# Performance work log

Measured on AMD Instinct MI355X. Metric: run time of the kernel, lower is better.

Reference implementation:

```python
import jax, jax.numpy as jnp
import numpy as np

B, T, D = 4, 2048, 1024
H, DK, DV = 16, 64, 64


def setup_inputs() -> dict:
    key = jax.random.key(0)
    ks = jax.random.split(key, 12)
    std = 1.0 / np.sqrt(D)
    inp = {
        "query": jax.random.normal(ks[0], (B, T, D), jnp.float32),
        "key": jax.random.normal(ks[1], (B, T, D), jnp.float32),
        "value": jax.random.normal(ks[2], (B, T, D), jnp.float32),
        "mask": jnp.ones((B, 1, 1, T), dtype=bool),
        # weights stored as [in, out] (torch Linear applies x @ W.T + b)
        "Wq": jax.random.truncated_normal(ks[3], -2, 2, (D, H * DK), jnp.float32) * std,
        "bq": jnp.zeros((H * DK,), jnp.float32),
        "Wk": jax.random.truncated_normal(ks[4], -2, 2, (D, H * DK), jnp.float32) * std,
        "bk": jnp.zeros((H * DK,), jnp.float32),
        "Wv": jax.random.truncated_normal(ks[5], -2, 2, (D, H * DV), jnp.float32) * std,
        "bv": jnp.zeros((H * DV,), jnp.float32),
        "Wo": jax.random.truncated_normal(ks[6], -2, 2, (H * DV, D), jnp.float32) * (1.0 / np.sqrt(H * DV)),
        "bo": jnp.zeros((D,), jnp.float32),
    }
    return inp


def reference(query, key, value, mask, Wq, bq, Wk, bk, Wv, bv, Wo, bo):
    denom = 1.0 / np.sqrt(DK)
    q = (query @ Wq + bq).reshape(B, T, H, DK)
    k = (key @ Wk + bk).reshape(B, T, H, DK)
    v = (value @ Wv + bv).reshape(B, T, H, DV)
    # [B, H, T, T] attention logits
    logits = jnp.einsum("bthd,bThd->bhtT", q, k) * denom
    logits = jnp.where(mask, logits, -1e30)
    w = jax.nn.softmax(logits, axis=-1)
    attn = jnp.einsum("bhtT,bThd->bthd", w, v).reshape(B, T, H * DV)
    return attn @ Wo + bo
```

## Files before the change

kernel.cpp:

```cpp
#include <hip/hip_runtime.h>


typedef _Float16 f16;
typedef f16 f16x4 __attribute__((ext_vector_type(4)));
typedef f16 f16x8 __attribute__((ext_vector_type(8)));
typedef __fp16 h16x2 __attribute__((ext_vector_type(2)));
typedef float f32x4 __attribute__((ext_vector_type(4)));
typedef float f32x16 __attribute__((ext_vector_type(16)));

__device__ __forceinline__ void gload_lds16(const void* g, void* l) {
  __builtin_amdgcn_global_load_lds(
      (const __attribute__((address_space(1))) unsigned int*)g,
      (__attribute__((address_space(3))) unsigned int*)l, 16, 0, 0);
}

__device__ __forceinline__ unsigned pku(float a, float b) {
  h16x2 p = __builtin_amdgcn_cvt_pkrtz(a, b);
  return __builtin_bit_cast(unsigned, p);
}

__device__ __forceinline__ f16x8 cvt8(const f32x4& a, const f32x4& b) {
  union { unsigned u[4]; f16x8 v; } m;
  m.u[0] = pku(a[0], a[1]);
  m.u[1] = pku(a[2], a[3]);
  m.u[2] = pku(b[0], b[1]);
  m.u[3] = pku(b[2], b[3]);
  return m.v;
}

__global__ __launch_bounds__(256) void wtrans4(const float* __restrict__ W0,
                                               const float* __restrict__ W1,
                                               const float* __restrict__ W2,
                                               const float* __restrict__ W3,
                                               f16* __restrict__ D0,
                                               f16* __restrict__ D1,
                                               f16* __restrict__ D2,
                                               f16* __restrict__ D3) {
  __shared__ float tile[32][33];
  const float* W;
  f16* D;
  switch (blockIdx.z) {
    case 0: W = W0; D = D0; break;
    case 1: W = W1; D = D1; break;
    case 2: W = W2; D = D2; break;
    default: W = W3; D = D3; break;
  }
  int tx = threadIdx.x, ty = threadIdx.y;
  int o0 = blockIdx.x * 32, i0 = blockIdx.y * 32;
#pragma unroll
  for (int r = 0; r < 32; r += 8)
    tile[ty + r][tx] = W[(size_t)(i0 + ty + r) * 1024 + o0 + tx];
  __syncthreads();
#pragma unroll
  for (int r = 0; r < 32; r += 8)
    D[(size_t)(o0 + ty + r) * 1024 + i0 + tx] = (f16)tile[tx][ty + r];
}

__global__ __launch_bounds__(256) void gemm_proj(
    const float* __restrict__ Aq, const float* __restrict__ Ak,
    const float* __restrict__ Av, const f16* __restrict__ WTq,
    const f16* __restrict__ WTk, const f16* __restrict__ WTv,
    const float* __restrict__ bq, const float* __restrict__ bk,
    const float* __restrict__ bv, f16* __restrict__ QB, f16* __restrict__ KB,
    f16* __restrict__ VT) {
  constexpr int N = 1024, K = 1024;
  constexpr int BM = 128, BK = 32;
  __shared__ f16 As[BM * BK];
  __shared__ f16 Bs[BM * BK];

  const int big = blockIdx.x;
  const int seg = big >> 9;
  const int bid = big & 511;
  const float* A;
  const f16* Bt;
  const float* bias;
  f16* C;
  if (seg == 0) { A = Aq; Bt = WTq; bias = bq; C = QB; }
  else if (seg == 1) { A = Ak; Bt = WTk; bias = bk; C = KB; }
  else { A = Av; Bt = WTv; bias = bv; C = VT; }
  const bool vmode = (seg == 2);

  const int t = threadIdx.x;
  int swz = (bid & 7) * 64 + (bid >> 3);
  const int tm = swz >> 3, tn = swz & 7;

  const int lane = t & 63, w = t >> 6;
  const int wr = w >> 1, wc = w & 1;
  const int lrow = lane & 15, kgrp = lane >> 4;

  f32x4 zero4 = {0.f, 0.f, 0.f, 0.f};
  f32x4 acc[4][4];
#pragma unroll
  for (int mi = 0; mi < 4; ++mi)
#pragma unroll
    for (int ni = 0; ni < 4; ++ni) acc[mi][ni] = zero4;

  const int srow = t >> 2;
  const int scol = (t & 3) * 8;
  const float* Ag32 = A + (size_t)(tm * BM + srow) * K + scol;
  const f16* Bg = Bt + (size_t)(tn * BM + srow) * K + scol;
  f16* Asl = &As[t * 8];
  f16* Bsl = &Bs[t * 8];

  f32x4 ar[4];
  auto loadA = [&](int k0) {
    ar[0] = *(const f32x4*)(Ag32 + k0);
    ar[1] = *(const f32x4*)(Ag32 + k0 + 4);
    ar[2] = *(const f32x4*)(Ag32 + (size_t)64 * K + k0);
    ar[3] = *(const f32x4*)(Ag32 + (size_t)64 * K + k0 + 4);
  };

  loadA(0);
  for (int k0 = 0; k0 < K; k0 += BK) {
    __syncthreads();
    *(f16x8*)Asl = cvt8(ar[0], ar[1]);
    *(f16x8*)(Asl + 64 * BK) = cvt8(ar[2], ar[3]);
    gload_lds16(Bg + k0, Bsl);
    gload_lds16(Bg + k0 + (size_t)64 * K, Bsl + 64 * BK);
    __syncthreads();
    if (k0 + BK < K) loadA(k0 + BK);

    f16x8 af[4], bf[4];
#pragma unroll
    for (int mi = 0; mi < 4; ++mi)
      af[mi] = *(const f16x8*)&As[(wr * 64 + mi * 16 + lrow) * BK + kgrp * 8];
#pragma unroll
    for (int ni = 0; ni < 4; ++ni)
      bf[ni] = *(const f16x8*)&Bs[(wc * 64 + ni * 16 + lrow) * BK + kgrp * 8];
#pragma unroll
    for (int mi = 0; mi < 4; ++mi)
#pragma unroll
      for (int ni = 0; ni < 4; ++ni)
        acc[mi][ni] = __builtin_amdgcn_mfma_f32_16x16x32_f16(af[mi], bf[ni],
                                                             acc[mi][ni], 0, 0, 0);
  }

#pragma unroll
  for (int mi = 0; mi < 4; ++mi) {
#pragma unroll
    for (int ni = 0; ni < 4; ++ni) {
      int col = tn * BM + wc * 64 + ni * 16 + lrow;
      float bv_ = bias[col];
#pragma unroll
      for (int j = 0; j < 4; ++j) {
        int row = tm * BM + wr * 64 + mi * 16 + kgrp * 4 + j;
        float v = acc[mi][ni][j] + bv_;
        if (vmode) {
          int bb = row >> 11, tt = row & 2047;
          C[((size_t)(bb * 1024 + col)) * 2048 + tt] = (f16)v;
        } else {
          C[(size_t)row * N + col] = (f16)v;
        }
      }
    }
  }
}

__global__ __launch_bounds__(256) void gemm_out(const f16* __restrict__ A,
                                                const f16* __restrict__ Bt,
                                                const float* __restrict__ bias,
                                                float* __restrict__ C32) {
  constexpr int N = 1024, K = 1024;
  constexpr int BM = 128, BK = 32;
  __shared__ f16 As[BM * BK];
  __shared__ f16 Bs[BM * BK];

  const int t = threadIdx.x;
  int bid = blockIdx.x;
  int swz = (bid & 7) * 64 + (bid >> 3);
  const int tm = swz >> 3, tn = swz & 7;

  const int lane = t & 63, w = t >> 6;
  const int wr = w >> 1, wc = w & 1;
  const int lrow = lane & 15, kgrp = lane >> 4;

  f32x4 zero4 = {0.f, 0.f, 0.f, 0.f};
  f32x4 acc[4][4];
#pragma unroll
  for (int mi = 0; mi < 4; ++mi)
#pragma unroll
    for (int ni = 0; ni < 4; ++ni) acc[mi][ni] = zero4;

  const int srow = t >> 2;
  const int scol = (t & 3) * 8;
  const f16* Ag = A + (size_t)(tm * BM + srow) * K + scol;
  const f16* Bg = Bt + (size_t)(tn * BM + srow) * K + scol;
  f16* Asl = &As[t * 8];
  f16* Bsl = &Bs[t * 8];

  for (int k0 = 0; k0 < K; k0 += BK) {
    __syncthreads();
    gload_lds16(Ag + k0, Asl);
    gload_lds16(Ag + k0 + (size_t)64 * K, Asl + 64 * BK);
    gload_lds16(Bg + k0, Bsl);
    gload_lds16(Bg + k0 + (size_t)64 * K, Bsl + 64 * BK);
    __syncthreads();

    f16x8 af[4], bf[4];
#pragma unroll
    for (int mi = 0; mi < 4; ++mi)
      af[mi] = *(const f16x8*)&As[(wr * 64 + mi * 16 + lrow) * BK + kgrp * 8];
#pragma unroll
    for (int ni = 0; ni < 4; ++ni)
      bf[ni] = *(const f16x8*)&Bs[(wc * 64 + ni * 16 + lrow) * BK + kgrp * 8];
#pragma unroll
    for (int mi = 0; mi < 4; ++mi)
#pragma unroll
      for (int ni = 0; ni < 4; ++ni)
        acc[mi][ni] = __builtin_amdgcn_mfma_f32_16x16x32_f16(af[mi], bf[ni],
                                                             acc[mi][ni], 0, 0, 0);
  }

#pragma unroll
  for (int mi = 0; mi < 4; ++mi) {
#pragma unroll
    for (int ni = 0; ni < 4; ++ni) {
      int col = tn * BM + wc * 64 + ni * 16 + lrow;
      float bv = bias[col];
#pragma unroll
      for (int j = 0; j < 4; ++j) {
        int row = tm * BM + wr * 64 + mi * 16 + kgrp * 4 + j;
        C32[(size_t)row * N + col] = acc[mi][ni][j] + bv;
      }
    }
  }
}

__global__ __launch_bounds__(256) void attn_fwd(const f16* __restrict__ Q,
                                                const f16* __restrict__ Kc,
                                                const f16* __restrict__ Vt,
                                                f16* __restrict__ O) {
  constexpr int T = 2048, HD = 1024;
  __shared__ __align__(16) f16 lds[16384];
  char* LB = (char*)lds;

  const int t = threadIdx.x;
  const int lane = t & 63, w = t >> 6;
  const int q5 = lane & 31, hi = lane >> 5;
  const int r7 = q5 & 7;
  int bid = blockIdx.x;
  int swzb = (bid & 7) * 128 + (bid >> 3);
  const int qt = swzb & 15, h = (swzb >> 4) & 15, b = swzb >> 8;

  f16x8 aq[4];
  {
    const f16* qp =
        Q + (size_t)(b * T + qt * 128 + w * 32 + q5) * HD + h * 64 + hi * 8;
#pragma unroll
    for (int s = 0; s < 4; ++s)
      aq[s] = (*(const f16x8*)(qp + s * 16)) * (f16)0.18033688f;
  }

  float m_r = -INFINITY, l_r = 0.f;
  f32x16 z16 = {0.f};
  f32x16 oa0 = z16, oa1 = z16;

  unsigned koff[4];
#pragma unroll
  for (int s = 0; s < 4; ++s)
    koff[s] = q5 * 128 + (((2 * s + hi) ^ r7) << 4);

  const int l8 = lane & 7, lr8 = lane >> 3;
  const int cs = (l8 ^ lr8) * 8;
  const f16* kg0 = Kc + (size_t)(b * T + w * 16 + lr8) * HD + h * 64 + cs;
  const f16* kg1 = kg0 + (size_t)8 * HD;
  const f16* vg0 = Vt + (size_t)(b * 1024 + h * 64 + w * 16 + lr8) * T + cs;
  const f16* vg1 = vg0 + (size_t)8 * T;
  const unsigned dsto = w * 2048 + lane * 16;

  auto stage = [&](unsigned sb) {
    gload_lds16(kg0, LB + sb + dsto);
    gload_lds16(kg1, LB + sb + dsto + 1024);
    gload_lds16(vg0, LB + 16384 + sb + dsto);
    gload_lds16(vg1, LB + 16384 + sb + dsto + 1024);
    kg0 += (size_t)64 * HD; kg1 += (size_t)64 * HD;
    vg0 += 64; vg1 += 64;
  };

  auto mk = [&](float e0, float e1, float e2, float e3, float e4, float e5,
                float e6, float e7) -> f16x8 {
    unsigned A01 = pku(e0, e1), A23 = pku(e2, e3);
    unsigned B01 = pku(e4, e5), B23 = pku(e6, e7);
    unsigned X0 = hi ? A01 : B01;
    unsigned X1 = hi ? A23 : B23;
    unsigned R0 = (unsigned)__shfl_xor((int)X0, 32, 64);
    unsigned R1 = (unsigned)__shfl_xor((int)X1, 32, 64);
    union { unsigned u[4]; f16x8 v; } m;
    m.u[0] = hi ? R0 : A01;
    m.u[1] = hi ? R1 : A23;
    m.u[2] = hi ? B01 : R0;
    m.u[3] = hi ? B23 : R1;
    return m.v;
  };

  auto body = [&](unsigned rb, unsigned sb, bool doStage) {
    if (doStage) stage(sb);

    f32x16 s0 = z16, s1 = z16;
    __builtin_amdgcn_s_setprio(1);
#pragma unroll
    for (int s = 0; s < 4; ++s) {
      f16x8 ka = *(const f16x8*)(LB + (rb + koff[s]));
      f16x8 kb = *(const f16x8*)(LB + (rb + 4096 + koff[s]));
      s0 = __builtin_amdgcn_mfma_f32_32x32x16_f16(ka, aq[s], s0, 0, 0, 0);
      s1 = __builtin_amdgcn_mfma_f32_32x32x16_f16(kb, aq[s], s1, 0, 0, 0);
    }
    __builtin_amdgcn_s_setprio(0);

    float a0 = fmaxf(fmaxf(s0[0], s0[1]), fmaxf(s0[2], s0[3]));
    float a1 = fmaxf(fmaxf(s0[4], s0[5]), fmaxf(s0[6], s0[7]));
    float a2 = fmaxf(fmaxf(s0[8], s0[9]), fmaxf(s0[10], s0[11]));
    float a3 = fmaxf(fmaxf(s0[12], s0[13]), fmaxf(s0[14], s0[15]));
    float a4 = fmaxf(fmaxf(s1[0], s1[1]), fmaxf(s1[2], s1[3]));
    float a5 = fmaxf(fmaxf(s1[4], s1[5]), fmaxf(s1[6], s1[7]));
    float a6 = fmaxf(fmaxf(s1[8], s1[9]), fmaxf(s1[10], s1[11]));
    float a7 = fmaxf(fmaxf(s1[12], s1[13]), fmaxf(s1[14], s1[15]));
    float mx = fmaxf(fmaxf(fmaxf(a0, a1), fmaxf(a2, a3)),
                     fmaxf(fmaxf(a4, a5), fmaxf(a6, a7)));
    mx = fmaxf(mx, __shfl_xor(mx, 32, 64));
    if (__any(mx > m_r + 8.f)) {
      float mnew = fmaxf(m_r, mx);
      float sc = exp2f(m_r - mnew);
      l_r *= sc;
      m_r = mnew;
#pragma unroll
      for (int i = 0; i < 16; ++i) { oa0[i] *= sc; oa1[i] *= sc; }
    }
#pragma unroll
    for (int i = 0; i < 16; ++i) s0[i] = exp2f(s0[i] - m_r);
#pragma unroll
    for (int i = 0; i < 16; ++i) s1[i] = exp2f(s1[i] - m_r);
    float r0 = ((s0[0] + s0[1]) + (s0[2] + s0[3])) +
               ((s0[4] + s0[5]) + (s0[6] + s0[7]));
    float r1 = ((s0[8] + s0[9]) + (s0[10] + s0[11])) +
               ((s0[12] + s0[13]) + (s0[14] + s0[15]));
    float r2 = ((s1[0] + s1[1]) + (s1[2] + s1[3])) +
               ((s1[4] + s1[5]) + (s1[6] + s1[7]));
    float r3 = ((s1[8] + s1[9]) + (s1[10] + s1[11])) +
               ((s1[12] + s1[13]) + (s1[14] + s1[15]));
    float rs = (r0 + r1) + (r2 + r3);
    rs += __shfl_xor(rs, 32, 64);
    l_r += rs;

    f16x8 pb0 = mk(s0[0], s0[1], s0[2], s0[3], s0[4], s0[5], s0[6], s0[7]);
    f16x8 pb1 = mk(s0[8], s0[9], s0[10], s0[11], s0[12], s0[13], s0[14], s0[15]);
    f16x8 pb2 = mk(s1[0], s1[1], s1[2], s1[3], s1[4], s1[5], s1[6], s1[7]);
    f16x8 pb3 = mk(s1[8], s1[9], s1[10], s1[11], s1[12], s1[13], s1[14], s1[15]);

    __builtin_amdgcn_s_setprio(1);
    {
      f16x8 v0 = *(const f16x8*)(LB + (16384 + rb + koff[0]));
      f16x8 v1 = *(const f16x8*)(LB + (16384 + rb + 4096 + koff[0]));
      oa0 = __builtin_amdgcn_mfma_f32_32x32x16_f16(v0, pb0, oa0, 0, 0, 0);
      oa1 = __builtin_amdgcn_mfma_f32_32x32x16_f16(v1, pb0, oa1, 0, 0, 0);
      v0 = *(const f16x8*)(LB + (16384 + rb + koff[1]));
      v1 = *(const f16x8*)(LB + (16384 + rb + 4096 + koff[1]));
      oa0 = __builtin_amdgcn_mfma_f32_32x32x16_f16(v0, pb1, oa0, 0, 0, 0);
      oa1 = __builtin_amdgcn_mfma_f32_32x32x16_f16(v1, pb1, oa1, 0, 0, 0);
      v0 = *(const f16x8*)(LB + (16384 + rb + koff[2]));
      v1 = *(const f16x8*)(LB + (16384 + rb + 4096 + koff[2]));
      oa0 = __builtin_amdgcn_mfma_f32_32x32x16_f16(v0, pb2, oa0, 0, 0, 0);
      oa1 = __builtin_amdgcn_mfma_f32_32x32x16_f16(v1, pb2, oa1, 0, 0, 0);
      v0 = *(const f16x8*)(LB + (16384 + rb + koff[3]));
      v1 = *(const f16x8*)(LB + (16384 + rb + 4096 + koff[3]));
      oa0 = __builtin_amdgcn_mfma_f32_32x32x16_f16(v0, pb3, oa0, 0, 0, 0);
      oa1 = __builtin_amdgcn_mfma_f32_32x32x16_f16(v1, pb3, oa1, 0, 0, 0);
    }
    __builtin_amdgcn_s_setprio(0);

    __syncthreads();
  };

  stage(0);
  __syncthreads();

#pragma unroll 1
  for (int i = 0; i < 15; ++i) {
    body(0, 8192, true);
    body(8192, 0, true);
  }
  body(0, 8192, true);
  body(8192, 0, false);

  float inv = 1.f / l_r;
  f16* orow = O + (size_t)(b * T + qt * 128 + w * 32 + q5) * HD + h * 64;
#pragma unroll
  for (int t2 = 0; t2 < 2; ++t2) {
    const f32x16& oa = t2 ? oa1 : oa0;
#pragma unroll
    for (int j = 0; j < 4; ++j) {
      f16x4 ov;
      ov[0] = (f16)(oa[4 * j + 0] * inv);
      ov[1] = (f16)(oa[4 * j + 1] * inv);
      ov[2] = (f16)(oa[4 * j + 2] * inv);
      ov[3] = (f16)(oa[4 * j + 3] * inv);
      *(f16x4*)(orow + t2 * 32 + j * 8 + hi * 4) = ov;
    }
  }
}

extern "C" void kernel_launch(void* const* d_in, const int* in_sizes, int n_in,
                              void* d_out, int out_size, void* d_ws, size_t ws_size,
                              hipStream_t stream) {
  (void)in_sizes; (void)n_in; (void)out_size; (void)ws_size;
  const float* query = (const float*)d_in[0];
  const float* key   = (const float*)d_in[1];
  const float* value = (const float*)d_in[2];
  const float* Wq = (const float*)d_in[4];
  const float* bq = (const float*)d_in[5];
  const float* Wk = (const float*)d_in[6];
  const float* bk = (const float*)d_in[7];
  const float* Wv = (const float*)d_in[8];
  const float* bv = (const float*)d_in[9];
  const float* Wo = (const float*)d_in[10];
  const float* bo = (const float*)d_in[11];
  float* out = (float*)d_out;

  f16* ws  = (f16*)d_ws;
  f16* WTq = ws;
  f16* WTk = WTq + 1048576;
  f16* WTv = WTk + 1048576;
  f16* WTo = WTv + 1048576;
  f16* QB  = WTo + 1048576;
  f16* KB  = QB + 8388608;
  f16* VT  = KB + 8388608;
  f16* AB  = VT + 8388608;

  wtrans4<<<dim3(32, 32, 4), dim3(32, 8), 0, stream>>>(Wq, Wk, Wv, Wo,
                                                       WTq, WTk, WTv, WTo);
  gemm_proj<<<dim3(1536), dim3(256), 0, stream>>>(query, key, value,
                                                  WTq, WTk, WTv,
                                                  bq, bk, bv, QB, KB, VT);
  attn_fwd<<<dim3(1024), dim3(256), 0, stream>>>(QB, KB, VT, AB);
  gemm_out<<<dim3(512), dim3(256), 0, stream>>>(AB, WTo, bo, out);
}
```

Measured before the change: 261.1 us.

## Widen attention blocks to 512 threads and compute row sums via MFMA

The attention kernel now runs 8 waves per block over 256 query rows, so each staged K/V tile in LDS is shared by twice as many waves, and each thread issues half as many global-to-LDS loads. The softmax row sum moves from VALU adds plus a cross-lane shuffle to an MFMA against a ones vector, which accumulates the sum in the matrix unit. Max reduction uses three-input max chains, and exp2 calls the raw hardware intrinsic. The costs are extra MFMA work per iteration, a 16-float accumulator for the sum, and half as many blocks in the grid.

New measurement: 222.7 us. 14.7% less time.

```diff
diff --git a/kernel.cpp b/kernel.cpp
--- a/kernel.cpp
+++ b/kernel.cpp
@@ -26,6 +26,13 @@
   m.u[2] = pku(b[0], b[1]);
   m.u[3] = pku(b[2], b[3]);
   return m.v;
+}
+
+__device__ __forceinline__ float e2(float x) {
+  return __builtin_amdgcn_exp2f(x);
+}
+__device__ __forceinline__ float m3(float a, float b, float c) {
+  return fmaxf(fmaxf(a, b), c);
 }
 
 __global__ __launch_bounds__(256) void wtrans4(const float* __restrict__ W0,
@@ -226,10 +233,10 @@
   }
 }
 
-__global__ __launch_bounds__(256) void attn_fwd(const f16* __restrict__ Q,
-                                                const f16* __restrict__ Kc,
-                                                const f16* __restrict__ Vt,
-                                                f16* __restrict__ O) {
+__global__ __launch_bounds__(512, 4) void attn_fwd(const f16* __restrict__ Q,
+                                                   const f16* __restrict__ Kc,
+                                                   const f16* __restrict__ Vt,
+                                                   f16* __restrict__ O) {
   constexpr int T = 2048, HD = 1024;
   __shared__ __align__(16) f16 lds[16384];
   char* LB = (char*)lds;
@@ -239,21 +246,26 @@
   const int q5 = lane & 31, hi = lane >> 5;
   const int r7 = q5 & 7;
   int bid = blockIdx.x;
-  int swzb = (bid & 7) * 128 + (bid >> 3);
-  const int qt = swzb & 15, h = (swzb >> 4) & 15, b = swzb >> 8;
+  int swzb = (bid & 7) * 64 + (bid >> 3);
+  const int qt = swzb & 7, h = (swzb >> 3) & 15, b = swzb >> 7;
 
   f16x8 aq[4];
   {
     const f16* qp =
-        Q + (size_t)(b * T + qt * 128 + w * 32 + q5) * HD + h * 64 + hi * 8;
+        Q + (size_t)(b * T + qt * 256 + w * 32 + q5) * HD + h * 64 + hi * 8;
 #pragma unroll
     for (int s = 0; s < 4; ++s)
       aq[s] = (*(const f16x8*)(qp + s * 16)) * (f16)0.18033688f;
   }
 
-  float m_r = -INFINITY, l_r = 0.f;
+  float m_r = -INFINITY;
   f32x16 z16 = {0.f};
   f32x16 oa0 = z16, oa1 = z16;
+  f32x16 la = z16;
+
+  f16x8 ones;
+#pragma unroll
+  for (int i = 0; i < 8; ++i) ones[i] = (f16)1.f;
 
   unsigned koff[4];
 #pragma unroll
@@ -262,19 +274,15 @@
 
   const int l8 = lane & 7, lr8 = lane >> 3;
   const int cs = (l8 ^ lr8) * 8;
-  const f16* kg0 = Kc + (size_t)(b * T + w * 16 + lr8) * HD + h * 64 + cs;
-  const f16* kg1 = kg0 + (size_t)8 * HD;
-  const f16* vg0 = Vt + (size_t)(b * 1024 + h * 64 + w * 16 + lr8) * T + cs;
-  const f16* vg1 = vg0 + (size_t)8 * T;
-  const unsigned dsto = w * 2048 + lane * 16;
+  const f16* kg = Kc + (size_t)(b * T + w * 8 + lr8) * HD + h * 64 + cs;
+  const f16* vg = Vt + (size_t)(b * 1024 + h * 64 + w * 8 + lr8) * T + cs;
+  const unsigned dbase = w * 1024;
 
   auto stage = [&](unsigned sb) {
-    gload_lds16(kg0, LB + sb + dsto);
-    gload_lds16(kg1, LB + sb + dsto + 1024);
-    gload_lds16(vg0, LB + 16384 + sb + dsto);
-    gload_lds16(vg1, LB + 16384 + sb + dsto + 1024);
-    kg0 += (size_t)64 * HD; kg1 += (size_t)64 * HD;
-    vg0 += 64; vg1 += 64;
+    gload_lds16(kg, LB + sb + dbase);
+    gload_lds16(vg, LB + 16384 + sb + dbase);
+    kg += (size_t)64 * HD;
+    vg += 64;
   };
 
   auto mk = [&](float e0, float e1, float e2, float e3, float e4, float e5,
@@ -307,40 +315,33 @@
     }
     __builtin_amdgcn_s_setprio(0);
 
-    float a0 = fmaxf(fmaxf(s0[0], s0[1]), fmaxf(s0[2], s0[3]));
-    float a1 = fmaxf(fmaxf(s0[4], s0[5]), fmaxf(s0[6], s0[7]));
-    float a2 = fmaxf(fmaxf(s0[8], s0[9]), fmaxf(s0[10], s0[11]));
-    float a3 = fmaxf(fmaxf(s0[12], s0[13]), fmaxf(s0[14], s0[15]));
-    float a4 = fmaxf(fmaxf(s1[0], s1[1]), fmaxf(s1[2], s1[3]));
-    float a5 = fmaxf(fmaxf(s1[4], s1[5]), fmaxf(s1[6], s1[7]));
-    float a6 = fmaxf(fmaxf(s1[8], s1[9]), fmaxf(s1[10], s1[11]));
-    float a7 = fmaxf(fmaxf(s1[12], s1[13]), fmaxf(s1[14], s1[15]));
-    float mx = fmaxf(fmaxf(fmaxf(a0, a1), fmaxf(a2, a3)),
-                     fmaxf(fmaxf(a4, a5), fmaxf(a6, a7)));
+    float c0 = m3(s0[0], s0[1], s0[2]);
+    c0 = m3(c0, s0[3], s0[4]);
+    c0 = m3(c0, s0[5], s0[6]);
+    float c1 = m3(s0[8], s0[9], s0[10]);
+    c1 = m3(c1, s0[11], s0[12]);
+    c1 = m3(c1, s0[13], s0[14]);
+    float c2 = m3(s1[0], s1[1], s1[2]);
+    c2 = m3(c2, s1[3], s1[4]);
+    c2 = m3(c2, s1[5], s1[6]);
+    float c3 = m3(s1[8], s1[9], s1[10]);
+    c3 = m3(c3, s1[11], s1[12]);
+    c3 = m3(c3, s1[13], s1[14]);
+    c0 = m3(c0, s0[7], s0[15]);
+    c1 = m3(c1, s1[7], s1[15]);
+    float mx = m3(c0, c1, m3(c2, c3, m_r));
     mx = fmaxf(mx, __shfl_xor(mx, 32, 64));
     if (__any(mx > m_r + 8.f)) {
-      float mnew = fmaxf(m_r, mx);
-      float sc = exp2f(m_r - mnew);
-      l_r *= sc;
-      m_r = mnew;
+      float sc = e2(m_r - mx);
+      m_r = mx;
+      la[0] *= sc;
 #pragma unroll
       for (int i = 0; i < 16; ++i) { oa0[i] *= sc; oa1[i] *= sc; }
     }
 #pragma unroll
-    for (int i = 0; i < 16; ++i) s0[i] = exp2f(s0[i] - m_r);
-#pragma unroll
-    for (int i = 0; i < 16; ++i) s1[i] = exp2f(s1[i] - m_r);
-    float r0 = ((s0[0] + s0[1]) + (s0[2] + s0[3])) +
-               ((s0[4] + s0[5]) + (s0[6] + s0[7]));
-    float r1 = ((s0[8] + s0[9]) + (s0[10] + s0[11])) +
-               ((s0[12] + s0[13]) + (s0[14] + s0[15]));
-    float r2 = ((s1[0] + s1[1]) + (s1[2] + s1[3])) +
-               ((s1[4] + s1[5]) + (s1[6] + s1[7]));
-    float r3 = ((s1[8] + s1[9]) + (s1[10] + s1[11])) +
-               ((s1[12] + s1[13]) + (s1[14] + s1[15]));
-    float rs = (r0 + r1) + (r2 + r3);
-    rs += __shfl_xor(rs, 32, 64);
-    l_r += rs;
+    for (int i = 0; i < 16; ++i) s0[i] = e2(s0[i] - m_r);
+#pragma unroll
+    for (int i = 0; i < 16; ++i) s1[i] = e2(s1[i] - m_r);
 
     f16x8 pb0 = mk(s0[0], s0[1], s0[2], s0[3], s0[4], s0[5], s0[6], s0[7]);
     f16x8 pb1 = mk(s0[8], s0[9], s0[10], s0[11], s0[12], s0[13], s0[14], s0[15]);
@@ -348,6 +349,10 @@
     f16x8 pb3 = mk(s1[8], s1[9], s1[10], s1[11], s1[12], s1[13], s1[14], s1[15]);
 
     __builtin_amdgcn_s_setprio(1);
+    la = __builtin_amdgcn_mfma_f32_32x32x16_f16(ones, pb0, la, 0, 0, 0);
+    la = __builtin_amdgcn_mfma_f32_32x32x16_f16(ones, pb1, la, 0, 0, 0);
+    la = __builtin_amdgcn_mfma_f32_32x32x16_f16(ones, pb2, la, 0, 0, 0);
+    la = __builtin_amdgcn_mfma_f32_32x32x16_f16(ones, pb3, la, 0, 0, 0);
     {
       f16x8 v0 = *(const f16x8*)(LB + (16384 + rb + koff[0]));
       f16x8 v1 = *(const f16x8*)(LB + (16384 + rb + 4096 + koff[0]));
@@ -382,8 +387,8 @@
   body(0, 8192, true);
   body(8192, 0, false);
 
-  float inv = 1.f / l_r;
-  f16* orow = O + (size_t)(b * T + qt * 128 + w * 32 + q5) * HD + h * 64;
+  float inv = 1.f / la[0];
+  f16* orow = O + (size_t)(b * T + qt * 256 + w * 32 + q5) * HD + h * 64;
 #pragma unroll
   for (int t2 = 0; t2 < 2; ++t2) {
     const f32x16& oa = t2 ? oa1 : oa0;
@@ -431,6 +436,6 @@
   gemm_proj<<<dim3(1536), dim3(256), 0, stream>>>(query, key, value,
                                                   WTq, WTk, WTv,
                                                   bq, bk, bv, QB, KB, VT);
-  attn_fwd<<<dim3(1024), dim3(256), 0, stream>>>(QB, KB, VT, AB);
+  attn_fwd<<<dim3(512), dim3(512), 0, stream>>>(QB, KB, VT, AB);
   gemm_out<<<dim3(512), dim3(256), 0, stream>>>(AB, WTo, bo, out);
 }
```
